# Kernel optimization log

Hardware: AMD Instinct MI355X
Metric: run time of the kernel (lower is better)

## Reference

```python
import jax, jax.numpy as jnp
import numpy as np

EPS = 1e-05
QN, QP = -128.0, 127.0


def setup_inputs() -> dict:
    key = jax.random.key(0)
    kx, kw = jax.random.split(key)
    x = jax.random.normal(kx, (4, 2048, 4096), dtype=jnp.float32)
    weight = jax.random.normal(kw, (4096, 4096), dtype=jnp.float32)  # [out, in]
    return {"x": x, "weight": weight}


def reference(x, weight):
    # --- per-token int8 activation quantization (activation_quant) ---
    # s: [B, S, 1], scale so that max(|x|) maps to 127
    s = QP / jnp.clip(jnp.max(jnp.abs(x), axis=-1, keepdims=True), 1e-05, None)
    q = jnp.clip(jnp.round(x * s), QN, QP)  # int8-valued, kept in float
    xq = q / s  # dequantized activations fed to the matmul

    # --- ternary weight quantization (terniarize + pack/unpack round-trip) ---
    scale_w = 1.0 / jnp.clip(jnp.mean(jnp.abs(weight)), EPS, None)
    tw = jnp.clip(jnp.round(weight * scale_w), -1.0, 1.0)  # ternary {-1,0,1}, [out, in]

    # --- bitmat: (xq) @ tw^T, then dequant by weight scale ---
    out = jnp.einsum('bsi,oi->bso', xq, tw) / scale_w
    return out
```

## Files before the change

### kernel.cpp

```cpp
#include <hip/hip_runtime.h>
#include <stdint.h>

#define K_DIM 4096
#define M_TOK 8192
#define N_OUT 4096

typedef int v4i __attribute__((ext_vector_type(4)));


__device__ __forceinline__ void gload_lds16(const void* g, void* l) {
    auto gp = reinterpret_cast<const __attribute__((address_space(1))) uint32_t*>(
        reinterpret_cast<uintptr_t>(g));
    auto lp = reinterpret_cast<__attribute__((address_space(3))) uint32_t*>(
        reinterpret_cast<uintptr_t>(l));
    __builtin_amdgcn_global_load_lds(gp, lp, 16, 0, 0);
}

__global__ __launch_bounds__(256) void quant_act(const float* __restrict__ x,
                                                 int8_t* __restrict__ q,
                                                 float* __restrict__ rs,
                                                 double* __restrict__ acc) {
    const int token = blockIdx.x;
    const int t = threadIdx.x;
    if (token == 0 && t == 0) *acc = 0.0;
    const float4* x4 = (const float4*)(x + (size_t)token * K_DIM);
    float4 v[4];
    float m = 0.0f;
#pragma unroll
    for (int r = 0; r < 4; ++r) {
        v[r] = x4[t + 256 * r];
        m = fmaxf(m, fmaxf(fmaxf(fabsf(v[r].x), fabsf(v[r].y)),
                           fmaxf(fabsf(v[r].z), fabsf(v[r].w))));
    }
#pragma unroll
    for (int off = 32; off; off >>= 1) m = fmaxf(m, __shfl_down(m, off, 64));
    __shared__ float wmax[4];
    __shared__ float smax;
    if ((t & 63) == 0) wmax[t >> 6] = m;
    __syncthreads();
    if (t == 0) smax = fmaxf(fmaxf(wmax[0], wmax[1]), fmaxf(wmax[2], wmax[3]));
    __syncthreads();
    const float s = 127.0f / fmaxf(smax, 1e-5f);
    char4* q4 = (char4*)(q + (size_t)token * K_DIM);
#pragma unroll
    for (int r = 0; r < 4; ++r) {
        float4 f = v[r];
        char4 c;
        c.x = (signed char)fminf(fmaxf(rintf(f.x * s), -128.0f), 127.0f);
        c.y = (signed char)fminf(fmaxf(rintf(f.y * s), -128.0f), 127.0f);
        c.z = (signed char)fminf(fmaxf(rintf(f.z * s), -128.0f), 127.0f);
        c.w = (signed char)fminf(fmaxf(rintf(f.w * s), -128.0f), 127.0f);
        q4[t + 256 * r] = c;
    }
    if (t == 0) rs[token] = 1.0f / s;
}

__global__ __launch_bounds__(256) void wabs_sum(const float* __restrict__ w,
                                                double* __restrict__ acc) {
    const size_t n4 = (size_t)N_OUT * K_DIM / 4;
    const size_t stride = (size_t)gridDim.x * 256;
    const float4* w4 = (const float4*)w;
    float sum = 0.0f;
    for (size_t j = (size_t)blockIdx.x * 256 + threadIdx.x; j < n4; j += stride) {
        float4 f = w4[j];
        sum += fabsf(f.x) + fabsf(f.y) + fabsf(f.z) + fabsf(f.w);
    }
    double d = (double)sum;
#pragma unroll
    for (int off = 32; off; off >>= 1) d += __shfl_down(d, off, 64);
    __shared__ double wsum[4];
    const int t = threadIdx.x;
    if ((t & 63) == 0) wsum[t >> 6] = d;
    __syncthreads();
    if (t == 0) atomicAdd(acc, wsum[0] + wsum[1] + wsum[2] + wsum[3]);
}

__global__ __launch_bounds__(256) void ternarize(const float* __restrict__ w,
                                                 int8_t* __restrict__ tw,
                                                 const double* __restrict__ acc) {
    const double mean = *acc * (1.0 / ((double)N_OUT * (double)K_DIM));
    const float sw = 1.0f / fmaxf((float)mean, 1e-5f);
    const size_t i = (size_t)blockIdx.x * 256 + threadIdx.x;
    const float4* w4 = (const float4*)w;
    char4* t4 = (char4*)tw;
    float4 f = w4[i];
    char4 c;
    c.x = (signed char)fminf(fmaxf(rintf(f.x * sw), -1.0f), 1.0f);
    c.y = (signed char)fminf(fmaxf(rintf(f.y * sw), -1.0f), 1.0f);
    c.z = (signed char)fminf(fmaxf(rintf(f.z * sw), -1.0f), 1.0f);
    c.w = (signed char)fminf(fmaxf(rintf(f.w * sw), -1.0f), 1.0f);
    t4[i] = c;
}

__global__ __launch_bounds__(512) void gemm_i8(const int8_t* __restrict__ A,
                                               const int8_t* __restrict__ B,
                                               const float* __restrict__ rs,
                                               const double* __restrict__ acc,
                                               float* __restrict__ out) {
    const int bm = blockIdx.y * 256;
    const int bn = blockIdx.x * 256;
    __shared__ int8_t As[256 * 64];
    __shared__ int8_t Bs[256 * 64];
    const int t = threadIdx.x;
    const int lane = t & 63;
    const int wave = t >> 6;
    const int wm = (wave >> 1) * 64;
    const int wn = (wave & 1) * 128;

    v4i accv[4][8] = {};

    const int srow = t >> 2;
    const int scol = (((t & 3) ^ ((t >> 3) & 3)) << 4);
    const int8_t* Ag0 = A + (size_t)(bm + srow) * K_DIM + scol;
    const int8_t* Ag1 = Ag0 + (size_t)128 * K_DIM;
    const int8_t* Bg0 = B + (size_t)(bn + srow) * K_DIM + scol;
    const int8_t* Bg1 = Bg0 + (size_t)128 * K_DIM;
    int8_t* lA0 = As + t * 16;
    int8_t* lA1 = As + 8192 + t * 16;
    int8_t* lB0 = Bs + t * 16;
    int8_t* lB1 = Bs + 8192 + t * 16;

    const int fr = lane & 15;
    const int sw16 = (((lane >> 4) ^ ((fr >> 1) & 3)) << 4);

    for (int k0 = 0; k0 < K_DIM; k0 += 64) {
        gload_lds16(Ag0 + k0, lA0);
        gload_lds16(Ag1 + k0, lA1);
        gload_lds16(Bg0 + k0, lB0);
        gload_lds16(Bg1 + k0, lB1);
        __syncthreads();

        v4i af[4], bf[8];
#pragma unroll
        for (int i = 0; i < 4; ++i)
            af[i] = *(const v4i*)(As + (wm + i * 16 + fr) * 64 + sw16);
#pragma unroll
        for (int j = 0; j < 8; ++j)
            bf[j] = *(const v4i*)(Bs + (wn + j * 16 + fr) * 64 + sw16);
#pragma unroll
        for (int i = 0; i < 4; ++i)
#pragma unroll
            for (int j = 0; j < 8; ++j)
                accv[i][j] = __builtin_amdgcn_mfma_i32_16x16x64_i8(af[i], bf[j], accv[i][j], 0, 0, 0);
        __syncthreads();
    }

    const double mean = *acc * (1.0 / ((double)N_OUT * (double)K_DIM));
    const float wmean = fmaxf((float)mean, 1e-5f);
    const int crow0 = (lane >> 4) * 4;
    const int ccol = lane & 15;
#pragma unroll
    for (int i = 0; i < 4; ++i) {
        const int rbase = bm + wm + i * 16 + crow0;
#pragma unroll
        for (int reg = 0; reg < 4; ++reg) {
            const int r = rbase + reg;
            const float scale = rs[r] * wmean;
            float* orow = out + (size_t)r * N_OUT + bn + wn + ccol;
#pragma unroll
            for (int j = 0; j < 8; ++j)
                orow[j * 16] = (float)accv[i][j][reg] * scale;
        }
    }
}

extern "C" void kernel_launch(void* const* d_in, const int* in_sizes, int n_in,
                              void* d_out, int out_size, void* d_ws, size_t ws_size,
                              hipStream_t stream) {
    const float* x = (const float*)d_in[0];
    const float* w = (const float*)d_in[1];
    float* out = (float*)d_out;
    char* ws = (char*)d_ws;
    int8_t* q = (int8_t*)ws;
    int8_t* tw = (int8_t*)(ws + 33554432);
    float* rs = (float*)(ws + 50331648);
    double* acc = (double*)(ws + 50364416);

    hipLaunchKernelGGL(quant_act, dim3(M_TOK), dim3(256), 0, stream, x, q, rs, acc);
    hipLaunchKernelGGL(wabs_sum, dim3(2048), dim3(256), 0, stream, w, acc);
    hipLaunchKernelGGL(ternarize, dim3((N_OUT * (size_t)K_DIM / 4) / 256), dim3(256), 0, stream, w, tw, acc);
    hipLaunchKernelGGL(gemm_i8, dim3(N_OUT / 256, M_TOK / 256), dim3(512), 0, stream, q, tw, rs, acc, out);
}
```

Before: 441.6 us.

## Fuse quant and weight-sum kernels, double-buffer B and load A directly to registers

Activation quantization and the weight abs-sum now run in one launch, and the weight sum goes into per-block partials instead of atomics. The ternarize kernel reduces those partials itself and writes out the weight mean. In the GEMM, A fragments are loaded straight from global memory into registers and prefetched one K step ahead. B is double-buffered in LDS so there is one barrier per iteration instead of two. The cost is uncoalesced direct global A loads and higher register pressure from the prefetched fragments.

```diff
diff --git a/kernel.cpp b/kernel.cpp
--- a/kernel.cpp
+++ b/kernel.cpp
@@ -16,137 +16,156 @@
     __builtin_amdgcn_global_load_lds(gp, lp, 16, 0, 0);
 }
 
-__global__ __launch_bounds__(256) void quant_act(const float* __restrict__ x,
-                                                 int8_t* __restrict__ q,
-                                                 float* __restrict__ rs,
-                                                 double* __restrict__ acc) {
-    const int token = blockIdx.x;
+__global__ __launch_bounds__(256) void prep(const float* __restrict__ x,
+                                            const float* __restrict__ w,
+                                            int8_t* __restrict__ q,
+                                            float* __restrict__ rs,
+                                            double* __restrict__ partial) {
+    const int b = blockIdx.x;
     const int t = threadIdx.x;
-    if (token == 0 && t == 0) *acc = 0.0;
-    const float4* x4 = (const float4*)(x + (size_t)token * K_DIM);
-    float4 v[4];
-    float m = 0.0f;
-#pragma unroll
-    for (int r = 0; r < 4; ++r) {
-        v[r] = x4[t + 256 * r];
-        m = fmaxf(m, fmaxf(fmaxf(fabsf(v[r].x), fabsf(v[r].y)),
-                           fmaxf(fabsf(v[r].z), fabsf(v[r].w))));
-    }
-#pragma unroll
-    for (int off = 32; off; off >>= 1) m = fmaxf(m, __shfl_down(m, off, 64));
-    __shared__ float wmax[4];
-    __shared__ float smax;
-    if ((t & 63) == 0) wmax[t >> 6] = m;
-    __syncthreads();
-    if (t == 0) smax = fmaxf(fmaxf(wmax[0], wmax[1]), fmaxf(wmax[2], wmax[3]));
-    __syncthreads();
-    const float s = 127.0f / fmaxf(smax, 1e-5f);
-    char4* q4 = (char4*)(q + (size_t)token * K_DIM);
-#pragma unroll
-    for (int r = 0; r < 4; ++r) {
-        float4 f = v[r];
-        char4 c;
-        c.x = (signed char)fminf(fmaxf(rintf(f.x * s), -128.0f), 127.0f);
-        c.y = (signed char)fminf(fmaxf(rintf(f.y * s), -128.0f), 127.0f);
-        c.z = (signed char)fminf(fmaxf(rintf(f.z * s), -128.0f), 127.0f);
-        c.w = (signed char)fminf(fmaxf(rintf(f.w * s), -128.0f), 127.0f);
-        q4[t + 256 * r] = c;
-    }
-    if (t == 0) rs[token] = 1.0f / s;
-}
-
-__global__ __launch_bounds__(256) void wabs_sum(const float* __restrict__ w,
-                                                double* __restrict__ acc) {
-    const size_t n4 = (size_t)N_OUT * K_DIM / 4;
-    const size_t stride = (size_t)gridDim.x * 256;
-    const float4* w4 = (const float4*)w;
-    float sum = 0.0f;
-    for (size_t j = (size_t)blockIdx.x * 256 + threadIdx.x; j < n4; j += stride) {
-        float4 f = w4[j];
-        sum += fabsf(f.x) + fabsf(f.y) + fabsf(f.z) + fabsf(f.w);
-    }
-    double d = (double)sum;
-#pragma unroll
-    for (int off = 32; off; off >>= 1) d += __shfl_down(d, off, 64);
-    __shared__ double wsum[4];
-    const int t = threadIdx.x;
-    if ((t & 63) == 0) wsum[t >> 6] = d;
-    __syncthreads();
-    if (t == 0) atomicAdd(acc, wsum[0] + wsum[1] + wsum[2] + wsum[3]);
+    if (b < M_TOK) {
+        const float4* x4 = (const float4*)(x + (size_t)b * K_DIM);
+        float4 v[4];
+        float m = 0.0f;
+#pragma unroll
+        for (int r = 0; r < 4; ++r) {
+            v[r] = x4[t + 256 * r];
+            m = fmaxf(m, fmaxf(fmaxf(fabsf(v[r].x), fabsf(v[r].y)),
+                               fmaxf(fabsf(v[r].z), fabsf(v[r].w))));
+        }
+#pragma unroll
+        for (int off = 32; off; off >>= 1) m = fmaxf(m, __shfl_down(m, off, 64));
+        __shared__ float wmax[4];
+        __shared__ float smax;
+        if ((t & 63) == 0) wmax[t >> 6] = m;
+        __syncthreads();
+        if (t == 0) smax = fmaxf(fmaxf(wmax[0], wmax[1]), fmaxf(wmax[2], wmax[3]));
+        __syncthreads();
+        const float s = 127.0f / fmaxf(smax, 1e-5f);
+        char4* q4 = (char4*)(q + (size_t)b * K_DIM);
+#pragma unroll
+        for (int r = 0; r < 4; ++r) {
+            float4 f = v[r];
+            char4 c;
+            c.x = (signed char)fminf(fmaxf(rintf(f.x * s), -128.0f), 127.0f);
+            c.y = (signed char)fminf(fmaxf(rintf(f.y * s), -128.0f), 127.0f);
+            c.z = (signed char)fminf(fmaxf(rintf(f.z * s), -128.0f), 127.0f);
+            c.w = (signed char)fminf(fmaxf(rintf(f.w * s), -128.0f), 127.0f);
+            q4[t + 256 * r] = c;
+        }
+        if (t == 0) rs[b] = 1.0f / s;
+    } else {
+        const int wb = b - M_TOK;
+        const float4* w4 = (const float4*)w + (size_t)wb * 16384 + t;
+        double sum = 0.0;
+#pragma unroll 8
+        for (int r = 0; r < 64; ++r) {
+            float4 f = w4[(size_t)r * 256];
+            sum += (double)(fabsf(f.x) + fabsf(f.y)) + (double)(fabsf(f.z) + fabsf(f.w));
+        }
+#pragma unroll
+        for (int off = 32; off; off >>= 1) sum += __shfl_down(sum, off, 64);
+        __shared__ double dsum[4];
+        if ((t & 63) == 0) dsum[t >> 6] = sum;
+        __syncthreads();
+        if (t == 0) partial[wb] = dsum[0] + dsum[1] + dsum[2] + dsum[3];
+    }
 }
 
 __global__ __launch_bounds__(256) void ternarize(const float* __restrict__ w,
                                                  int8_t* __restrict__ tw,
-                                                 const double* __restrict__ acc) {
-    const double mean = *acc * (1.0 / ((double)N_OUT * (double)K_DIM));
-    const float sw = 1.0f / fmaxf((float)mean, 1e-5f);
-    const size_t i = (size_t)blockIdx.x * 256 + threadIdx.x;
+                                                 const double* __restrict__ partial,
+                                                 float* __restrict__ wmean_out) {
+    const int t = threadIdx.x;
+    double d = partial[t];
+#pragma unroll
+    for (int off = 32; off; off >>= 1) d += __shfl_down(d, off, 64);
+    __shared__ double sh[4];
+    __shared__ float swsh;
+    if ((t & 63) == 0) sh[t >> 6] = d;
+    __syncthreads();
+    if (t == 0) {
+        double mean = (sh[0] + sh[1] + sh[2] + sh[3]) * (1.0 / ((double)N_OUT * (double)K_DIM));
+        float wm = fmaxf((float)mean, 1e-5f);
+        swsh = 1.0f / wm;
+        if (blockIdx.x == 0) *wmean_out = wm;
+    }
+    __syncthreads();
+    const float sw = swsh;
     const float4* w4 = (const float4*)w;
     char4* t4 = (char4*)tw;
-    float4 f = w4[i];
-    char4 c;
-    c.x = (signed char)fminf(fmaxf(rintf(f.x * sw), -1.0f), 1.0f);
-    c.y = (signed char)fminf(fmaxf(rintf(f.y * sw), -1.0f), 1.0f);
-    c.z = (signed char)fminf(fmaxf(rintf(f.z * sw), -1.0f), 1.0f);
-    c.w = (signed char)fminf(fmaxf(rintf(f.w * sw), -1.0f), 1.0f);
-    t4[i] = c;
+    const size_t base = (size_t)blockIdx.x * 1024 + t;
+#pragma unroll
+    for (int r = 0; r < 4; ++r) {
+        float4 f = w4[base + 256 * r];
+        char4 c;
+        c.x = (signed char)fminf(fmaxf(rintf(f.x * sw), -1.0f), 1.0f);
+        c.y = (signed char)fminf(fmaxf(rintf(f.y * sw), -1.0f), 1.0f);
+        c.z = (signed char)fminf(fmaxf(rintf(f.z * sw), -1.0f), 1.0f);
+        c.w = (signed char)fminf(fmaxf(rintf(f.w * sw), -1.0f), 1.0f);
+        t4[base + 256 * r] = c;
+    }
 }
 
 __global__ __launch_bounds__(512) void gemm_i8(const int8_t* __restrict__ A,
                                                const int8_t* __restrict__ B,
                                                const float* __restrict__ rs,
-                                               const double* __restrict__ acc,
+                                               const float* __restrict__ wmean_p,
                                                float* __restrict__ out) {
     const int bm = blockIdx.y * 256;
     const int bn = blockIdx.x * 256;
-    __shared__ int8_t As[256 * 64];
-    __shared__ int8_t Bs[256 * 64];
+    __shared__ int8_t Bs[2][256 * 64];
     const int t = threadIdx.x;
     const int lane = t & 63;
     const int wave = t >> 6;
     const int wm = (wave >> 1) * 64;
     const int wn = (wave & 1) * 128;
+    const int fr = lane & 15;
+    const int kq = lane >> 4;
 
     v4i accv[4][8] = {};
 
     const int srow = t >> 2;
     const int scol = (((t & 3) ^ ((t >> 3) & 3)) << 4);
-    const int8_t* Ag0 = A + (size_t)(bm + srow) * K_DIM + scol;
-    const int8_t* Ag1 = Ag0 + (size_t)128 * K_DIM;
     const int8_t* Bg0 = B + (size_t)(bn + srow) * K_DIM + scol;
     const int8_t* Bg1 = Bg0 + (size_t)128 * K_DIM;
-    int8_t* lA0 = As + t * 16;
-    int8_t* lA1 = As + 8192 + t * 16;
-    int8_t* lB0 = Bs + t * 16;
-    int8_t* lB1 = Bs + 8192 + t * 16;
-
-    const int fr = lane & 15;
-    const int sw16 = (((lane >> 4) ^ ((fr >> 1) & 3)) << 4);
-
+
+    const int8_t* Arow0 = A + (size_t)(bm + wm + fr) * K_DIM + kq * 16;
+
+    const int co = ((kq ^ ((fr >> 1) & 3)) << 4);
+
+    gload_lds16(Bg0, &Bs[0][t * 16]);
+    gload_lds16(Bg1, &Bs[0][8192 + t * 16]);
+    v4i af[4], afn[4];
+#pragma unroll
+    for (int i = 0; i < 4; ++i)
+        af[i] = *(const v4i*)(Arow0 + (size_t)(i * 16) * K_DIM);
+
+    int buf = 0;
     for (int k0 = 0; k0 < K_DIM; k0 += 64) {
-        gload_lds16(Ag0 + k0, lA0);
-        gload_lds16(Ag1 + k0, lA1);
-        gload_lds16(Bg0 + k0, lB0);
-        gload_lds16(Bg1 + k0, lB1);
-        __syncthreads();
-
-        v4i af[4], bf[8];
-#pragma unroll
-        for (int i = 0; i < 4; ++i)
-            af[i] = *(const v4i*)(As + (wm + i * 16 + fr) * 64 + sw16);
+        __syncthreads();
+        if (k0 + 64 < K_DIM) {
+            gload_lds16(Bg0 + k0 + 64, &Bs[buf ^ 1][t * 16]);
+            gload_lds16(Bg1 + k0 + 64, &Bs[buf ^ 1][8192 + t * 16]);
+#pragma unroll
+            for (int i = 0; i < 4; ++i)
+                afn[i] = *(const v4i*)(Arow0 + (size_t)(i * 16) * K_DIM + k0 + 64);
+        }
+        v4i bf[8];
 #pragma unroll
         for (int j = 0; j < 8; ++j)
-            bf[j] = *(const v4i*)(Bs + (wn + j * 16 + fr) * 64 + sw16);
+            bf[j] = *(const v4i*)(&Bs[buf][(wn + j * 16 + fr) * 64 + co]);
 #pragma unroll
         for (int i = 0; i < 4; ++i)
 #pragma unroll
             for (int j = 0; j < 8; ++j)
                 accv[i][j] = __builtin_amdgcn_mfma_i32_16x16x64_i8(af[i], bf[j], accv[i][j], 0, 0, 0);
-        __syncthreads();
-    }
-
-    const double mean = *acc * (1.0 / ((double)N_OUT * (double)K_DIM));
-    const float wmean = fmaxf((float)mean, 1e-5f);
+#pragma unroll
+        for (int i = 0; i < 4; ++i) af[i] = afn[i];
+        buf ^= 1;
+    }
+
+    const float wmean = wmean_p[0];
     const int crow0 = (lane >> 4) * 4;
     const int ccol = lane & 15;
 #pragma unroll
@@ -174,10 +193,10 @@
     int8_t* q = (int8_t*)ws;
     int8_t* tw = (int8_t*)(ws + 33554432);
     float* rs = (float*)(ws + 50331648);
-    double* acc = (double*)(ws + 50364416);
-
-    hipLaunchKernelGGL(quant_act, dim3(M_TOK), dim3(256), 0, stream, x, q, rs, acc);
-    hipLaunchKernelGGL(wabs_sum, dim3(2048), dim3(256), 0, stream, w, acc);
-    hipLaunchKernelGGL(ternarize, dim3((N_OUT * (size_t)K_DIM / 4) / 256), dim3(256), 0, stream, w, tw, acc);
-    hipLaunchKernelGGL(gemm_i8, dim3(N_OUT / 256, M_TOK / 256), dim3(512), 0, stream, q, tw, rs, acc, out);
-}
+    double* partial = (double*)(ws + 50364416);
+    float* wmean = (float*)(ws + 50366464);
+
+    hipLaunchKernelGGL(prep, dim3(M_TOK + 256), dim3(256), 0, stream, x, w, q, rs, partial);
+    hipLaunchKernelGGL(ternarize, dim3(4096), dim3(256), 0, stream, w, tw, partial, wmean);
+    hipLaunchKernelGGL(gemm_i8, dim3(N_OUT / 256, M_TOK / 256), dim3(512), 0, stream, q, tw, rs, wmean, out);
+}
```

Result: slower. 462.4 us (+4.7%).
